# Kernel optimization log

Hardware: AMD Instinct MI355X
Metric: run time of the kernel (lower is better)

Reference implementation:

```python
import jax, jax.numpy as jnp
import numpy as np

NC, NP_, E = 100000, 50000, 500000
DC, DP = 256, 128
HID, OUT = 64, 64
H1, H2 = 2, 1
SLOPE = 0.2


def setup_inputs() -> dict:
    key = jax.random.key(0)
    ks = jax.random.split(key, 32)
    d = {}
    d['x_customer'] = jax.random.normal(ks[0], (NC, DC), jnp.float32)
    d['x_product'] = jax.random.normal(ks[1], (NP_, DP), jnp.float32)
    d['edge_src'] = jax.random.randint(ks[2], (E,), 0, NC, jnp.int32)
    d['edge_dst'] = jax.random.randint(ks[3], (E,), 0, NP_, jnp.int32)
    s = 0.1
    # layer1, edge type (customer, buys, product): src=customer, dst=product
    d['w1b_src'] = jax.random.normal(ks[4], (DC, H1 * HID)) * s
    d['w1b_dst'] = jax.random.normal(ks[5], (DP, H1 * HID)) * s
    d['a1b_src'] = jax.random.normal(ks[6], (H1, HID)) * s
    d['a1b_dst'] = jax.random.normal(ks[7], (H1, HID)) * s
    d['b1b'] = jnp.zeros((H1 * HID,), jnp.float32)
    # layer1, edge type (product, rev_buys, customer): src=product, dst=customer
    d['w1r_src'] = jax.random.normal(ks[8], (DP, H1 * HID)) * s
    d['w1r_dst'] = jax.random.normal(ks[9], (DC, H1 * HID)) * s
    d['a1r_src'] = jax.random.normal(ks[10], (H1, HID)) * s
    d['a1r_dst'] = jax.random.normal(ks[11], (H1, HID)) * s
    d['b1r'] = jnp.zeros((H1 * HID,), jnp.float32)
    # layer2 (input dim = H1*HID = 128 for both node types), heads=1
    d['w2b_src'] = jax.random.normal(ks[12], (H1 * HID, H2 * OUT)) * s
    d['w2b_dst'] = jax.random.normal(ks[13], (H1 * HID, H2 * OUT)) * s
    d['a2b_src'] = jax.random.normal(ks[14], (H2, OUT)) * s
    d['a2b_dst'] = jax.random.normal(ks[15], (H2, OUT)) * s
    d['b2b'] = jnp.zeros((H2 * OUT,), jnp.float32)
    d['w2r_src'] = jax.random.normal(ks[16], (H1 * HID, H2 * OUT)) * s
    d['w2r_dst'] = jax.random.normal(ks[17], (H1 * HID, H2 * OUT)) * s
    d['a2r_src'] = jax.random.normal(ks[18], (H2, OUT)) * s
    d['a2r_dst'] = jax.random.normal(ks[19], (H2, OUT)) * s
    d['b2r'] = jnp.zeros((H2 * OUT,), jnp.float32)
    return d


def _gat_conv(h_src, h_dst, e_src, e_dst, att_src, att_dst, bias, n_dst):
    # h_src: [Ns,H,C] projected source feats; h_dst: [Nd,H,C]
    a_s = (h_src * att_src).sum(-1)  # [Ns,H]
    a_d = (h_dst * att_dst).sum(-1)  # [Nd,H]
    alpha = jax.nn.leaky_relu(a_s[e_src] + a_d[e_dst], negative_slope=SLOPE)  # [E,H]
    m = jax.lax.stop_gradient(jax.ops.segment_max(alpha, e_dst, num_segments=n_dst))
    ex = jnp.exp(alpha - m[e_dst])
    den = jax.ops.segment_sum(ex, e_dst, num_segments=n_dst)
    w = ex / (den[e_dst] + 1e-16)  # segment softmax over incoming edges
    msg = h_src[e_src] * w[..., None]  # [E,H,C]
    out = jax.ops.segment_sum(msg, e_dst, num_segments=n_dst)  # [Nd,H,C]
    return out.reshape(n_dst, -1) + bias


def reference(x_customer, x_product, edge_src, edge_dst,
              w1b_src, w1b_dst, a1b_src, a1b_dst, b1b,
              w1r_src, w1r_dst, a1r_src, a1r_dst, b1r,
              w2b_src, w2b_dst, a2b_src, a2b_dst, b2b,
              w2r_src, w2r_dst, a2r_src, a2r_dst, b2r):
    # ---- layer 1 (heads=2, concat) ----
    hs = (x_customer @ w1b_src).reshape(NC, H1, HID)
    hd = (x_product @ w1b_dst).reshape(NP_, H1, HID)
    p1 = _gat_conv(hs, hd, edge_src, edge_dst, a1b_src, a1b_dst, b1b, NP_)
    hs = (x_product @ w1r_src).reshape(NP_, H1, HID)
    hd = (x_customer @ w1r_dst).reshape(NC, H1, HID)
    c1 = _gat_conv(hs, hd, edge_dst, edge_src, a1r_src, a1r_dst, b1r, NC)
    c1 = jax.nn.relu(c1)
    p1 = jax.nn.relu(p1)
    # ---- layer 2 (heads=1) ----
    hs = (c1 @ w2b_src).reshape(NC, H2, OUT)
    hd = (p1 @ w2b_dst).reshape(NP_, H2, OUT)
    p2 = _gat_conv(hs, hd, edge_src, edge_dst, a2b_src, a2b_dst, b2b, NP_)
    hs = (p1 @ w2r_src).reshape(NP_, H2, OUT)
    hd = (c1 @ w2r_dst).reshape(NC, H2, OUT)
    c2 = _gat_conv(hs, hd, edge_dst, edge_src, a2r_src, a2r_dst, b2r, NC)
    return c2, p2
```

## Files before the change

### kernel.cpp

```cpp
#include <hip/hip_runtime.h>
#include <hip/hip_bf16.h>

typedef __bf16 bf16_t;
typedef bf16_t bf16x2 __attribute__((ext_vector_type(2)));
typedef bf16_t bf16x4 __attribute__((ext_vector_type(4)));
typedef bf16_t bf16x8 __attribute__((ext_vector_type(8)));
typedef float f32x2 __attribute__((ext_vector_type(2)));
typedef float f32x4 __attribute__((ext_vector_type(4)));

static constexpr int NCn = 100000;
static constexpr int NPn = 50000;
static constexpr int NE  = 500000;

__device__ __forceinline__ float ldin(const void* p, size_t i, int fp32) {
    return fp32 ? ((const float*)p)[i] : (float)((const bf16_t*)p)[i];
}

__global__ __launch_bounds__(256) void prep_meta(const void* x, int* flag,
                                                 const void* w1bd, const void* a1bd,
                                                 const void* w1rd, const void* a1rd,
                                                 const void* w2bd, const void* a2bd,
                                                 const void* w2rd, const void* a2rd,
                                                 float* V1bd, float* V1rd,
                                                 float* V2bd, float* V2rd) {
    __shared__ int sflag;
    int t = threadIdx.x;
    if (t < 64) {
        const bf16_t* xb = (const bf16_t*)x;
        int bad = 0;
        for (int i = t; i < 512; i += 64) {
            float v = (float)xb[i];
            if (!(v > -1e4f && v < 1e4f)) bad = 1;
        }
        unsigned long long m = __ballot(bad);
        if (t == 0) { sflag = (m != 0ull) ? 1 : 0; flag[0] = sflag; }
    }
    __syncthreads();
    int fp32 = sflag;
    for (int idx = t; idx < 256; idx += 256) {
        int k = idx >> 1, h = idx & 1;
        float s = 0.f;
        for (int c = 0; c < 64; ++c)
            s += ldin(w1bd, (size_t)k * 128 + h * 64 + c, fp32) * ldin(a1bd, h * 64 + c, fp32);
        V1bd[k * 2 + h] = s;
    }
    for (int idx = t; idx < 512; idx += 256) {
        int k = idx >> 1, h = idx & 1;
        float s = 0.f;
        for (int c = 0; c < 64; ++c)
            s += ldin(w1rd, (size_t)k * 128 + h * 64 + c, fp32) * ldin(a1rd, h * 64 + c, fp32);
        V1rd[k * 2 + h] = s;
    }
    for (int k = t; k < 128; k += 256) {
        float s = 0.f;
        for (int c = 0; c < 64; ++c)
            s += ldin(w2bd, (size_t)k * 64 + c, fp32) * ldin(a2bd, c, fp32);
        V2bd[k] = s;
    }
    for (int k = t; k < 128; k += 256) {
        float s = 0.f;
        for (int c = 0; c < 64; ++c)
            s += ldin(w2rd, (size_t)k * 64 + c, fp32) * ldin(a2rd, c, fp32);
        V2rd[k] = s;
    }
}

__global__ __launch_bounds__(256) void prep_w4(const void* __restrict__ w1b, bf16_t* __restrict__ Wt1b,
                                               const void* __restrict__ w1r, bf16_t* __restrict__ Wt1r,
                                               const void* __restrict__ w2b, bf16_t* __restrict__ Wt2b,
                                               const void* __restrict__ w2r, bf16_t* __restrict__ Wt2r,
                                               const int* __restrict__ flag) {
    int fp32 = flag[0];
    int b = blockIdx.x;
    const void* W; bf16_t* Wt; int N, ks, base;
    if (b < 128)      { W = w1b; Wt = Wt1b; N = 128; ks = 8; base = 0;   }
    else if (b < 192) { W = w1r; Wt = Wt1r; N = 128; ks = 7; base = 128; }
    else if (b < 224) { W = w2b; Wt = Wt2b; N = 64;  ks = 7; base = 192; }
    else              { W = w2r; Wt = Wt2r; N = 64;  ks = 7; base = 224; }
    int idx = (b - base) * 256 + threadIdx.x;
    int K = 1 << ks;
    int n = idx >> ks, k = idx & (K - 1);
    if (n < N) Wt[idx] = (bf16_t)ldin(W, (size_t)k * N + n, fp32);
}

template<int K>
__global__ __launch_bounds__(256) void cvt_rows(const void* __restrict__ X,
                                                bf16_t* __restrict__ Xb,
                                                const float* __restrict__ V,
                                                float* __restrict__ ad,
                                                int M, const int* __restrict__ flag) {
    constexpr int EPL = K / 64;
    int fp32 = flag[0];
    int wid = (blockIdx.x * 256 + threadIdx.x) >> 6;
    int lane = threadIdx.x & 63;
    if (wid >= M) return;
    size_t base = (size_t)wid * K + lane * EPL;
    float x[EPL];
    if constexpr (EPL == 4) {
        if (fp32) { f32x4 t = *(const f32x4*)((const float*)X + base);
#pragma unroll
            for (int j = 0; j < 4; ++j) x[j] = t[j];
        } else { bf16x4 t = *(const bf16x4*)((const bf16_t*)X + base);
#pragma unroll
            for (int j = 0; j < 4; ++j) x[j] = (float)t[j];
        }
        bf16x4 o;
#pragma unroll
        for (int j = 0; j < 4; ++j) o[j] = (bf16_t)x[j];
        *(bf16x4*)(Xb + base) = o;
    } else {
        if (fp32) { f32x2 t = *(const f32x2*)((const float*)X + base);
#pragma unroll
            for (int j = 0; j < 2; ++j) x[j] = t[j];
        } else { bf16x2 t = *(const bf16x2*)((const bf16_t*)X + base);
#pragma unroll
            for (int j = 0; j < 2; ++j) x[j] = (float)t[j];
        }
        bf16x2 o;
#pragma unroll
        for (int j = 0; j < 2; ++j) o[j] = (bf16_t)x[j];
        *(bf16x2*)(Xb + base) = o;
    }
    float a0 = 0.f, a1 = 0.f;
#pragma unroll
    for (int j = 0; j < EPL; ++j) {
        int k = lane * EPL + j;
        a0 += x[j] * V[k * 2];
        a1 += x[j] * V[k * 2 + 1];
    }
    for (int off = 32; off; off >>= 1) {
        a0 += __shfl_down(a0, off);
        a1 += __shfl_down(a1, off);
    }
    if (lane == 0) { ad[(size_t)wid * 2] = a0; ad[(size_t)wid * 2 + 1] = a1; }
}

__global__ __launch_bounds__(256) void zero2(int* __restrict__ a, int na,
                                             int* __restrict__ b, int nb) {
    int i = blockIdx.x * 256 + threadIdx.x;
    if (i < na) a[i] = 0;
    else if (i - na < nb) b[i - na] = 0;
}

__global__ __launch_bounds__(256) void hist2(const int* __restrict__ esrc,
                                             const int* __restrict__ edst,
                                             int* __restrict__ cntR,
                                             int* __restrict__ cntB, int E) {
    int e = blockIdx.x * 256 + threadIdx.x;
    if (e >= E) return;
    atomicAdd(&cntB[edst[e]], 1);
    atomicAdd(&cntR[esrc[e]], 1);
}

__global__ __launch_bounds__(256) void scan_blocks(const int* __restrict__ cnt,
                                                   int* __restrict__ rs,
                                                   int* __restrict__ bsum, int N) {
    int t = threadIdx.x, b = blockIdx.x;
    int base = b * 1024 + t * 4;
    int c[4];
#pragma unroll
    for (int k = 0; k < 4; ++k) { int i = base + k; c[k] = (i < N) ? cnt[i] : 0; }
    int tsum = c[0] + c[1] + c[2] + c[3];
    __shared__ int sd[256];
    sd[t] = tsum;
    __syncthreads();
    for (int off = 1; off < 256; off <<= 1) {
        int x = (t >= off) ? sd[t - off] : 0;
        __syncthreads();
        sd[t] += x;
        __syncthreads();
    }
    int run = sd[t] - tsum;
#pragma unroll
    for (int k = 0; k < 4; ++k) { int i = base + k; if (i < N) rs[i] = run; run += c[k]; }
    if (t == 255) bsum[b] = sd[255];
}

__global__ __launch_bounds__(128) void scan_bsum2(int* __restrict__ bsumB, int nbB,
                                                  int* __restrict__ bsumR, int nbR) {
    int* bsum = blockIdx.x ? bsumR : bsumB;
    int nb = blockIdx.x ? nbR : nbB;
    int t = threadIdx.x;
    __shared__ int sd[128];
    int v = (t < nb) ? bsum[t] : 0;
    sd[t] = v;
    __syncthreads();
    for (int off = 1; off < 128; off <<= 1) {
        int x = (t >= off) ? sd[t - off] : 0;
        __syncthreads();
        sd[t] += x;
        __syncthreads();
    }
    if (t < nb) bsum[t] = sd[t] - v;
}

__global__ __launch_bounds__(256) void scan_add2(int* __restrict__ rsB, const int* __restrict__ bsumB,
                                                 int NB, int* __restrict__ cntB,
                                                 int* __restrict__ rsR, const int* __restrict__ bsumR,
                                                 int NR, int* __restrict__ cntR, int E) {
    int i = blockIdx.x * 256 + threadIdx.x;
    if (i < NB) { int v = rsB[i] + bsumB[i >> 10]; rsB[i] = v; cntB[i] = v; }
    if (i < NR) { int v = rsR[i] + bsumR[i >> 10]; rsR[i] = v; cntR[i] = v; }
    if (i == 0) { rsB[NB] = E; rsR[NR] = E; }
}

__global__ __launch_bounds__(256) void scatter2(const int* __restrict__ esrc,
                                                const int* __restrict__ edst,
                                                int* __restrict__ curB, int* __restrict__ curR,
                                                int* __restrict__ srcsB, int* __restrict__ dstsB,
                                                int* __restrict__ srcsR, int* __restrict__ dstsR,
                                                int E) {
    int e = blockIdx.x * 256 + threadIdx.x;
    if (e >= E) return;
    int s = esrc[e], d = edst[e];
    int pb = atomicAdd(&curB[d], 1);
    srcsB[pb] = s; dstsB[pb] = d;
    int pr = atomicAdd(&curR[s], 1);
    srcsR[pr] = d; dstsR[pr] = s;
}

template<int K>
__global__ __launch_bounds__(256) void gemm_nl(const bf16_t* __restrict__ A,
                                               const bf16_t* __restrict__ Wt,
                                               bf16_t* __restrict__ C,
                                               const void* __restrict__ att,
                                               float* __restrict__ asout, int H,
                                               int M, int N,
                                               const int* __restrict__ flag) {
    const int w = threadIdx.x >> 6;
    const int lane = threadIdx.x & 63;
    const int lm = lane & 15;
    const int lq = lane >> 4;
    const int n0 = blockIdx.y * 64;
    const int r0 = blockIdx.x * 128 + w * 32;
    int ra0 = r0 + lm;       if (ra0 > M - 1) ra0 = M - 1;
    int ra1 = r0 + 16 + lm;  if (ra1 > M - 1) ra1 = M - 1;
    const bf16_t* A0 = A + (size_t)ra0 * K + lq * 8;
    const bf16_t* A1 = A + (size_t)ra1 * K + lq * 8;
    const bf16_t* B0 = Wt + (size_t)(n0 + lm) * K + lq * 8;
    f32x4 acc[2][4] = {};
#pragma unroll
    for (int kt = 0; kt < K / 32; ++kt) {
        bf16x8 a0 = *(const bf16x8*)(A0 + kt * 32);
        bf16x8 a1 = *(const bf16x8*)(A1 + kt * 32);
#pragma unroll
        for (int nt = 0; nt < 4; ++nt) {
            bf16x8 b = *(const bf16x8*)(B0 + (size_t)nt * 16 * K + kt * 32);
            acc[0][nt] = __builtin_amdgcn_mfma_f32_16x16x32_bf16(a0, b, acc[0][nt], 0, 0, 0);
            acc[1][nt] = __builtin_amdgcn_mfma_f32_16x16x32_bf16(a1, b, acc[1][nt], 0, 0, 0);
        }
    }
#pragma unroll
    for (int rt = 0; rt < 2; ++rt) {
        const int crow0 = r0 + rt * 16 + lq * 4;
#pragma unroll
        for (int nt = 0; nt < 4; ++nt) {
            int col = n0 + nt * 16 + lm;
#pragma unroll
            for (int i = 0; i < 4; ++i) {
                int r = crow0 + i;
                if (r < M) C[(size_t)r * N + col] = (bf16_t)acc[rt][nt][i];
            }
        }
    }
    int fp32 = flag[0];
    float attv[4];
#pragma unroll
    for (int nt = 0; nt < 4; ++nt) attv[nt] = ldin(att, n0 + nt * 16 + lm, fp32);
    float part[2][4];
#pragma unroll
    for (int rt = 0; rt < 2; ++rt)
#pragma unroll
        for (int i = 0; i < 4; ++i) {
            float s = 0.f;
#pragma unroll
            for (int nt = 0; nt < 4; ++nt) s += acc[rt][nt][i] * attv[nt];
            part[rt][i] = s;
        }
#pragma unroll
    for (int off = 1; off < 16; off <<= 1)
#pragma unroll
        for (int rt = 0; rt < 2; ++rt)
#pragma unroll
            for (int i = 0; i < 4; ++i)
                part[rt][i] += __shfl_xor(part[rt][i], off);
    if (lm == 0) {
#pragma unroll
        for (int rt = 0; rt < 2; ++rt)
#pragma unroll
            for (int i = 0; i < 4; ++i) {
                int r = r0 + rt * 16 + lq * 4 + i;
                if (r < M) asout[(size_t)r * H + blockIdx.y] = part[rt][i];
            }
    }
}

template<int H>
__global__ __launch_bounds__(256) void edge_ex2(const int* __restrict__ srcsB,
                                                const int* __restrict__ dstsB,
                                                const float* __restrict__ asB,
                                                const float* __restrict__ adB,
                                                float* __restrict__ exBp,
                                                const int* __restrict__ srcsR,
                                                const int* __restrict__ dstsR,
                                                const float* __restrict__ asR,
                                                const float* __restrict__ adR,
                                                float* __restrict__ exRp, int E) {
    int i = blockIdx.x * 256 + threadIdx.x;
    const int *srcs, *dsts; const float *as_, *ad_; float* ex; int j;
    if (i < E) { j = i; srcs = srcsB; dsts = dstsB; as_ = asB; ad_ = adB; ex = exBp; }
    else {
        j = i - E;
        if (j >= E) return;
        srcs = srcsR; dsts = dstsR; as_ = asR; ad_ = adR; ex = exRp;
    }
    int s = srcs[j], d = dsts[j];
    if constexpr (H == 2) {
        f32x2 a = *(const f32x2*)(as_ + 2 * (size_t)s);
        f32x2 b = *(const f32x2*)(ad_ + 2 * (size_t)d);
        float v0 = a[0] + b[0]; v0 = v0 > 0.f ? v0 : 0.2f * v0;
        float v1 = a[1] + b[1]; v1 = v1 > 0.f ? v1 : 0.2f * v1;
        f32x2 o;
        o[0] = __expf(fminf(v0, 60.f));
        o[1] = __expf(fminf(v1, 60.f));
        *(f32x2*)(ex + 2 * (size_t)j) = o;
    } else {
        float v = as_[s] + ad_[d];
        v = v > 0.f ? v : 0.2f * v;
        ex[j] = __expf(fminf(v, 60.f));
    }
}

template<int HD, int MODE>
__global__ __launch_bounds__(256) void aggregate2(
        const int* __restrict__ rsB, const int* __restrict__ srcsB,
        const float* __restrict__ exB, const bf16_t* __restrict__ HmB,
        const void* __restrict__ biasB, const float* __restrict__ V2B,
        float* __restrict__ ad2B, void* __restrict__ outB, size_t obaseB, int NdB,
        const int* __restrict__ rsR, const int* __restrict__ srcsR,
        const float* __restrict__ exR, const bf16_t* __restrict__ HmR,
        const void* __restrict__ biasR, const float* __restrict__ V2R,
        float* __restrict__ ad2R, void* __restrict__ outR, size_t obaseR, int NdR,
        const int* __restrict__ flag) {
    constexpr int NH = HD / 64;
    int gw = (blockIdx.x * 256 + threadIdx.x) >> 6;
    int lane = threadIdx.x & 63;
    const int* rs; const int* srcs; const float* ex; const bf16_t* Hm;
    const void* bias; const float* V2; float* ad2; void* outb; size_t obase; int wid;
    if (gw < NdB) {
        wid = gw;
        rs = rsB; srcs = srcsB; ex = exB; Hm = HmB; bias = biasB;
        V2 = V2B; ad2 = ad2B; outb = outB; obase = obaseB;
    } else {
        wid = gw - NdB;
        if (wid >= NdR) return;
        rs = rsR; srcs = srcsR; ex = exR; Hm = HmR; bias = biasR;
        V2 = V2R; ad2 = ad2R; outb = outR; obase = obaseR;
    }
    int start = rs[wid], end = rs[wid + 1];
    int fp32 = flag[0];
    const int hsel = lane >> 5;

    float den = 0.f, acc0 = 0.f, acc1 = 0.f;
#pragma unroll 4
    for (int j = start; j < end; ++j) {
        int s = srcs[j];
        if constexpr (NH == 2) {
            f32x2 e = *(const f32x2*)(ex + 2 * (size_t)j);
            float eh = hsel ? e[1] : e[0];
            den += eh;
            bf16x2 hv = *(const bf16x2*)(Hm + (size_t)s * 128 + 2 * lane);
            acc0 += (float)hv[0] * eh;
            acc1 += (float)hv[1] * eh;
        } else {
            float eh = ex[j];
            den += eh;
            acc0 += (float)Hm[(size_t)s * 64 + lane] * eh;
        }
    }
    float inv = 1.f / (den + 1e-16f);

    if constexpr (MODE == 0) {
        int c0 = 2 * lane;
        float o0 = fmaxf(acc0 * inv + ldin(bias, c0, fp32), 0.f);
        float o1 = fmaxf(acc1 * inv + ldin(bias, c0 + 1, fp32), 0.f);
        bf16x2 ov;
        ov[0] = (bf16_t)o0;
        ov[1] = (bf16_t)o1;
        *(bf16x2*)((bf16_t*)outb + (size_t)wid * 128 + c0) = ov;
        float pp = o0 * V2[c0] + o1 * V2[c0 + 1];
        for (int off = 32; off; off >>= 1) pp += __shfl_down(pp, off);
        if (lane == 0) ad2[wid] = pp;
    } else {
        float o = acc0 * inv + ldin(bias, lane, fp32);
        size_t oi = obase + (size_t)wid * 64 + lane;
        if (fp32) ((float*)outb)[oi] = o;
        else      ((bf16_t*)outb)[oi] = (bf16_t)o;
    }
}

extern "C" void kernel_launch(void* const* d_in, const int* in_sizes, int n_in,
                              void* d_out, int out_size, void* d_ws, size_t ws_size,
                              hipStream_t stream) {
    const void* xc = d_in[0];
    const void* xp = d_in[1];
    const int* esrc = (const int*)d_in[2];
    const int* edst = (const int*)d_in[3];
    const void* w1b_src = d_in[4];
    const void* w1b_dst = d_in[5];
    const void* a1b_src = d_in[6];
    const void* a1b_dst = d_in[7];
    const void* b1b     = d_in[8];
    const void* w1r_src = d_in[9];
    const void* w1r_dst = d_in[10];
    const void* a1r_src = d_in[11];
    const void* a1r_dst = d_in[12];
    const void* b1r     = d_in[13];
    const void* w2b_src = d_in[14];
    const void* w2b_dst = d_in[15];
    const void* a2b_src = d_in[16];
    const void* a2b_dst = d_in[17];
    const void* b2b     = d_in[18];
    const void* w2r_src = d_in[19];
    const void* w2r_dst = d_in[20];
    const void* a2r_src = d_in[21];
    const void* a2r_dst = d_in[22];
    const void* b2r     = d_in[23];

    char* p = (char*)d_ws;
    auto alloc = [&](size_t nbytes) {
        char* r = p;
        p += (nbytes + 255) & ~(size_t)255;
        return r;
    };
    int* flag   = (int*)alloc(256);
    float* V1bd = (float*)alloc(256 * 4);
    float* V1rd = (float*)alloc(512 * 4);
    float* V2bd = (float*)alloc(128 * 4);
    float* V2rd = (float*)alloc(128 * 4);
    bf16_t* Wt1b = (bf16_t*)alloc(128 * 256 * 2);
    bf16_t* Wt1r = (bf16_t*)alloc(128 * 128 * 2);
    bf16_t* Wt2b = (bf16_t*)alloc(64 * 128 * 2);
    bf16_t* Wt2r = (bf16_t*)alloc(64 * 128 * 2);
    float* as_b = (float*)alloc((size_t)NCn * 2 * 4);
    float* as_r = (float*)alloc((size_t)NPn * 2 * 4);
    float* as2_c = (float*)alloc((size_t)NCn * 4);
    float* as2_p = (float*)alloc((size_t)NPn * 4);
    float* ad_b = (float*)alloc((size_t)NPn * 2 * 4);
    float* ad_r = (float*)alloc((size_t)NCn * 2 * 4);
    float* ad2_b = (float*)alloc((size_t)NPn * 4);
    float* ad2_r = (float*)alloc((size_t)NCn * 4);
    int* rsB    = (int*)alloc((size_t)(NPn + 1) * 4);
    int* rsR    = (int*)alloc((size_t)(NCn + 1) * 4);
    int* srcsB  = (int*)alloc((size_t)NE * 4);
    int* srcsR  = (int*)alloc((size_t)NE * 4);
    int* dstsB  = (int*)alloc((size_t)NE * 4);
    int* dstsR  = (int*)alloc((size_t)NE * 4);
    float* exB  = (float*)alloc((size_t)NE * 2 * 4);
    float* exR  = (float*)alloc((size_t)NE * 2 * 4);
    int* cntB   = (int*)alloc((size_t)NPn * 4);
    int* cntR   = (int*)alloc((size_t)NCn * 4);
    int* bsumB  = (int*)alloc(128 * 4);
    int* bsumR  = (int*)alloc(128 * 4);
    bf16_t* xcb = (bf16_t*)alloc((size_t)NCn * 256 * 2);
    bf16_t* xpb = (bf16_t*)alloc((size_t)NPn * 128 * 2);
    bf16_t* Hc  = (bf16_t*)alloc((size_t)NCn * 128 * 2);
    bf16_t* Hp  = (bf16_t*)alloc((size_t)NPn * 128 * 2);
    bf16_t* c1  = (bf16_t*)alloc((size_t)NCn * 128 * 2);
    bf16_t* p1  = (bf16_t*)alloc((size_t)NPn * 128 * 2);
    bf16_t* Hc2 = (bf16_t*)alloc((size_t)NCn * 64 * 2);
    bf16_t* Hp2 = (bf16_t*)alloc((size_t)NPn * 64 * 2);

    const dim3 blk(256);
    const int gE = (NE + 255) / 256;
    const int g2E = (2 * NE + 255) / 256;
    const int sbP = (NPn + 1023) / 1024;
    const int sbR = (NCn + 1023) / 1024;
    const int gmC = (NCn + 127) / 128;
    const int gmP = (NPn + 127) / 128;
    const int gNC = (NCn + 255) / 256;
    const int gBoth = (NPn + NCn + 255) / 256;
    const int gAgg = (NPn + NCn + 3) / 4;

    prep_meta<<<1, 256, 0, stream>>>(xc, flag, w1b_dst, a1b_dst, w1r_dst, a1r_dst,
                                     w2b_dst, a2b_dst, w2r_dst, a2r_dst,
                                     V1bd, V1rd, V2bd, V2rd);
    prep_w4<<<256, blk, 0, stream>>>(w1b_src, Wt1b, w1r_src, Wt1r,
                                     w2b_src, Wt2b, w2r_src, Wt2r, flag);

    zero2<<<gBoth, blk, 0, stream>>>(cntB, NPn, cntR, NCn);
    hist2<<<gE, blk, 0, stream>>>(esrc, edst, cntR, cntB, NE);
    scan_blocks<<<sbP, blk, 0, stream>>>(cntB, rsB, bsumB, NPn);
    scan_blocks<<<sbR, blk, 0, stream>>>(cntR, rsR, bsumR, NCn);
    scan_bsum2<<<2, 128, 0, stream>>>(bsumB, sbP, bsumR, sbR);
    scan_add2<<<gNC, blk, 0, stream>>>(rsB, bsumB, NPn, cntB, rsR, bsumR, NCn, cntR, NE);
    scatter2<<<gE, blk, 0, stream>>>(esrc, edst, cntB, cntR, srcsB, dstsB, srcsR, dstsR, NE);

    cvt_rows<256><<<(NCn + 3) / 4, blk, 0, stream>>>(xc, xcb, V1rd, ad_r, NCn, flag);
    cvt_rows<128><<<(NPn + 3) / 4, blk, 0, stream>>>(xp, xpb, V1bd, ad_b, NPn, flag);

    gemm_nl<256><<<dim3(gmC, 2), blk, 0, stream>>>(xcb, Wt1b, Hc, a1b_src, as_b, 2, NCn, 128, flag);
    gemm_nl<128><<<dim3(gmP, 2), blk, 0, stream>>>(xpb, Wt1r, Hp, a1r_src, as_r, 2, NPn, 128, flag);

    edge_ex2<2><<<g2E, blk, 0, stream>>>(srcsB, dstsB, as_b, ad_b, exB,
                                         srcsR, dstsR, as_r, ad_r, exR, NE);
    aggregate2<128, 0><<<gAgg, blk, 0, stream>>>(
        rsB, srcsB, exB, Hc, b1b, V2bd, ad2_b, p1, 0, NPn,
        rsR, srcsR, exR, Hp, b1r, V2rd, ad2_r, c1, 0, NCn, flag);

    gemm_nl<128><<<dim3(gmC, 1), blk, 0, stream>>>(c1, Wt2b, Hc2, a2b_src, as2_c, 1, NCn, 64, flag);
    gemm_nl<128><<<dim3(gmP, 1), blk, 0, stream>>>(p1, Wt2r, Hp2, a2r_src, as2_p, 1, NPn, 64, flag);

    edge_ex2<1><<<g2E, blk, 0, stream>>>(srcsB, dstsB, as2_c, ad2_b, exB,
                                         srcsR, dstsR, as2_p, ad2_r, exR, NE);
    aggregate2<64, 1><<<gAgg, blk, 0, stream>>>(
        rsB, srcsB, exB, Hc2, b2b, nullptr, nullptr, d_out, (size_t)NCn * 64, NPn,
        rsR, srcsR, exR, Hp2, b2r, nullptr, nullptr, d_out, 0, NCn, flag);
}
```

Baseline: 622.9 us.

## Merge paired launches and pack source offsets with edge weights for aggregation

Paired kernels for the two edge types (scan, row conversion, layer-1 and layer-2 GEMMs) are merged into single launches that pick their branch from the block index, cutting launch count and tail idle time. The edge-weight pass now also writes the precomputed byte offset of each source row into a packed record next to the exp weights. Aggregation then reads one vector load per edge instead of separate srcs and ex loads. In exchange the packed buffer is larger (16 bytes per edge for two heads, including padding) and the offset is bit-cast into a float slot.

Result: faster. 598.1 us (-4.0%).

```diff
diff --git a/kernel.cpp b/kernel.cpp
--- a/kernel.cpp
+++ b/kernel.cpp
@@ -84,14 +84,13 @@
 }
 
 template<int K>
-__global__ __launch_bounds__(256) void cvt_rows(const void* __restrict__ X,
-                                                bf16_t* __restrict__ Xb,
-                                                const float* __restrict__ V,
-                                                float* __restrict__ ad,
-                                                int M, const int* __restrict__ flag) {
+__device__ __forceinline__ void cvt_body(const void* __restrict__ X,
+                                         bf16_t* __restrict__ Xb,
+                                         const float* __restrict__ V,
+                                         float* __restrict__ ad,
+                                         int M, int fp32, int blk) {
     constexpr int EPL = K / 64;
-    int fp32 = flag[0];
-    int wid = (blockIdx.x * 256 + threadIdx.x) >> 6;
+    int wid = (blk * 256 + (int)threadIdx.x) >> 6;
     int lane = threadIdx.x & 63;
     if (wid >= M) return;
     size_t base = (size_t)wid * K + lane * EPL;
@@ -133,6 +132,16 @@
         a1 += __shfl_down(a1, off);
     }
     if (lane == 0) { ad[(size_t)wid * 2] = a0; ad[(size_t)wid * 2 + 1] = a1; }
+}
+
+__global__ __launch_bounds__(256) void cvt2(const void* __restrict__ Xc, bf16_t* __restrict__ Xcb,
+                                            const float* __restrict__ Vc, float* __restrict__ adc,
+                                            const void* __restrict__ Xp, bf16_t* __restrict__ Xpb,
+                                            const float* __restrict__ Vp, float* __restrict__ adp,
+                                            int gC, const int* __restrict__ flag) {
+    int fp32 = flag[0];
+    if ((int)blockIdx.x < gC) cvt_body<256>(Xc, Xcb, Vc, adc, NCn, fp32, blockIdx.x);
+    else                      cvt_body<128>(Xp, Xpb, Vp, adp, NPn, fp32, blockIdx.x - gC);
 }
 
 __global__ __launch_bounds__(256) void zero2(int* __restrict__ a, int na,
@@ -152,10 +161,14 @@
     atomicAdd(&cntR[esrc[e]], 1);
 }
 
-__global__ __launch_bounds__(256) void scan_blocks(const int* __restrict__ cnt,
-                                                   int* __restrict__ rs,
-                                                   int* __restrict__ bsum, int N) {
-    int t = threadIdx.x, b = blockIdx.x;
+__global__ __launch_bounds__(256) void scan_blocks2(const int* __restrict__ cntB, int* __restrict__ rsB,
+                                                    int* __restrict__ bsumB, int NB, int sbB,
+                                                    const int* __restrict__ cntR, int* __restrict__ rsR,
+                                                    int* __restrict__ bsumR, int NR) {
+    const int* cnt; int* rs; int* bsum; int N; int b;
+    if ((int)blockIdx.x < sbB) { cnt = cntB; rs = rsB; bsum = bsumB; N = NB; b = blockIdx.x; }
+    else { cnt = cntR; rs = rsR; bsum = bsumR; N = NR; b = blockIdx.x - sbB; }
+    int t = threadIdx.x;
     int base = b * 1024 + t * 4;
     int c[4];
 #pragma unroll
@@ -220,19 +233,18 @@
 }
 
 template<int K>
-__global__ __launch_bounds__(256) void gemm_nl(const bf16_t* __restrict__ A,
-                                               const bf16_t* __restrict__ Wt,
-                                               bf16_t* __restrict__ C,
-                                               const void* __restrict__ att,
-                                               float* __restrict__ asout, int H,
-                                               int M, int N,
-                                               const int* __restrict__ flag) {
+__device__ __forceinline__ void gemm_body(const bf16_t* __restrict__ A,
+                                          const bf16_t* __restrict__ Wt,
+                                          bf16_t* __restrict__ C,
+                                          const void* __restrict__ att,
+                                          float* __restrict__ asout, int H,
+                                          int M, int N, int fp32, int bx, int by) {
     const int w = threadIdx.x >> 6;
     const int lane = threadIdx.x & 63;
     const int lm = lane & 15;
     const int lq = lane >> 4;
-    const int n0 = blockIdx.y * 64;
-    const int r0 = blockIdx.x * 128 + w * 32;
+    const int n0 = by * 64;
+    const int r0 = bx * 128 + w * 32;
     int ra0 = r0 + lm;       if (ra0 > M - 1) ra0 = M - 1;
     int ra1 = r0 + 16 + lm;  if (ra1 > M - 1) ra1 = M - 1;
     const bf16_t* A0 = A + (size_t)ra0 * K + lq * 8;
@@ -263,7 +275,6 @@
             }
         }
     }
-    int fp32 = flag[0];
     float attv[4];
 #pragma unroll
     for (int nt = 0; nt < 4; ++nt) attv[nt] = ldin(att, n0 + nt * 16 + lm, fp32);
@@ -290,29 +301,53 @@
 #pragma unroll
             for (int i = 0; i < 4; ++i) {
                 int r = r0 + rt * 16 + lq * 4 + i;
-                if (r < M) asout[(size_t)r * H + blockIdx.y] = part[rt][i];
+                if (r < M) asout[(size_t)r * H + by] = part[rt][i];
             }
     }
 }
 
+__global__ __launch_bounds__(256) void gemm_l1(const bf16_t* __restrict__ xcb, const bf16_t* __restrict__ Wt1b,
+                                               bf16_t* __restrict__ Hc, const void* __restrict__ a1b, float* __restrict__ as_b,
+                                               const bf16_t* __restrict__ xpb, const bf16_t* __restrict__ Wt1r,
+                                               bf16_t* __restrict__ Hp, const void* __restrict__ a1r, float* __restrict__ as_r,
+                                               int gmC, const int* __restrict__ flag) {
+    int fp32 = flag[0];
+    if ((int)blockIdx.x < gmC)
+        gemm_body<256>(xcb, Wt1b, Hc, a1b, as_b, 2, NCn, 128, fp32, blockIdx.x, blockIdx.y);
+    else
+        gemm_body<128>(xpb, Wt1r, Hp, a1r, as_r, 2, NPn, 128, fp32, blockIdx.x - gmC, blockIdx.y);
+}
+
+__global__ __launch_bounds__(256) void gemm_l2(const bf16_t* __restrict__ c1, const bf16_t* __restrict__ Wt2b,
+                                               bf16_t* __restrict__ Hc2, const void* __restrict__ a2b, float* __restrict__ as2c,
+                                               const bf16_t* __restrict__ p1, const bf16_t* __restrict__ Wt2r,
+                                               bf16_t* __restrict__ Hp2, const void* __restrict__ a2r, float* __restrict__ as2p,
+                                               int gmC, const int* __restrict__ flag) {
+    int fp32 = flag[0];
+    if ((int)blockIdx.x < gmC)
+        gemm_body<128>(c1, Wt2b, Hc2, a2b, as2c, 1, NCn, 64, fp32, blockIdx.x, 0);
+    else
+        gemm_body<128>(p1, Wt2r, Hp2, a2r, as2p, 1, NPn, 64, fp32, blockIdx.x - gmC, 0);
+}
+
 template<int H>
-__global__ __launch_bounds__(256) void edge_ex2(const int* __restrict__ srcsB,
+__global__ __launch_bounds__(256) void edge_pk2(const int* __restrict__ srcsB,
                                                 const int* __restrict__ dstsB,
                                                 const float* __restrict__ asB,
                                                 const float* __restrict__ adB,
-                                                float* __restrict__ exBp,
+                                                float* __restrict__ pkB,
                                                 const int* __restrict__ srcsR,
                                                 const int* __restrict__ dstsR,
                                                 const float* __restrict__ asR,
                                                 const float* __restrict__ adR,
-                                                float* __restrict__ exRp, int E) {
+                                                float* __restrict__ pkR, int E) {
     int i = blockIdx.x * 256 + threadIdx.x;
-    const int *srcs, *dsts; const float *as_, *ad_; float* ex; int j;
-    if (i < E) { j = i; srcs = srcsB; dsts = dstsB; as_ = asB; ad_ = adB; ex = exBp; }
+    const int *srcs, *dsts; const float *as_, *ad_; float* pk; int j;
+    if (i < E) { j = i; srcs = srcsB; dsts = dstsB; as_ = asB; ad_ = adB; pk = pkB; }
     else {
         j = i - E;
         if (j >= E) return;
-        srcs = srcsR; dsts = dstsR; as_ = asR; ad_ = adR; ex = exRp;
+        srcs = srcsR; dsts = dstsR; as_ = asR; ad_ = adR; pk = pkR;
     }
     int s = srcs[j], d = dsts[j];
     if constexpr (H == 2) {
@@ -320,41 +355,46 @@
         f32x2 b = *(const f32x2*)(ad_ + 2 * (size_t)d);
         float v0 = a[0] + b[0]; v0 = v0 > 0.f ? v0 : 0.2f * v0;
         float v1 = a[1] + b[1]; v1 = v1 > 0.f ? v1 : 0.2f * v1;
-        f32x2 o;
-        o[0] = __expf(fminf(v0, 60.f));
-        o[1] = __expf(fminf(v1, 60.f));
-        *(f32x2*)(ex + 2 * (size_t)j) = o;
+        f32x4 o;
+        o[0] = __uint_as_float((unsigned)s << 8);
+        o[1] = __expf(fminf(v0, 60.f));
+        o[2] = __expf(fminf(v1, 60.f));
+        o[3] = 0.f;
+        *(f32x4*)(pk + 4 * (size_t)j) = o;
     } else {
         float v = as_[s] + ad_[d];
         v = v > 0.f ? v : 0.2f * v;
-        ex[j] = __expf(fminf(v, 60.f));
+        f32x2 o;
+        o[0] = __uint_as_float((unsigned)s << 7);
+        o[1] = __expf(fminf(v, 60.f));
+        *(f32x2*)(pk + 2 * (size_t)j) = o;
     }
 }
 
 template<int HD, int MODE>
 __global__ __launch_bounds__(256) void aggregate2(
-        const int* __restrict__ rsB, const int* __restrict__ srcsB,
-        const float* __restrict__ exB, const bf16_t* __restrict__ HmB,
-        const void* __restrict__ biasB, const float* __restrict__ V2B,
-        float* __restrict__ ad2B, void* __restrict__ outB, size_t obaseB, int NdB,
-        const int* __restrict__ rsR, const int* __restrict__ srcsR,
-        const float* __restrict__ exR, const bf16_t* __restrict__ HmR,
-        const void* __restrict__ biasR, const float* __restrict__ V2R,
-        float* __restrict__ ad2R, void* __restrict__ outR, size_t obaseR, int NdR,
+        const int* __restrict__ rsB, const float* __restrict__ pkB,
+        const bf16_t* __restrict__ HmB, const void* __restrict__ biasB,
+        const float* __restrict__ V2B, float* __restrict__ ad2B,
+        void* __restrict__ outB, size_t obaseB, int NdB,
+        const int* __restrict__ rsR, const float* __restrict__ pkR,
+        const bf16_t* __restrict__ HmR, const void* __restrict__ biasR,
+        const float* __restrict__ V2R, float* __restrict__ ad2R,
+        void* __restrict__ outR, size_t obaseR, int NdR,
         const int* __restrict__ flag) {
     constexpr int NH = HD / 64;
     int gw = (blockIdx.x * 256 + threadIdx.x) >> 6;
     int lane = threadIdx.x & 63;
-    const int* rs; const int* srcs; const float* ex; const bf16_t* Hm;
+    const int* rs; const float* pk; const bf16_t* Hm;
     const void* bias; const float* V2; float* ad2; void* outb; size_t obase; int wid;
     if (gw < NdB) {
         wid = gw;
-        rs = rsB; srcs = srcsB; ex = exB; Hm = HmB; bias = biasB;
+        rs = rsB; pk = pkB; Hm = HmB; bias = biasB;
         V2 = V2B; ad2 = ad2B; outb = outB; obase = obaseB;
     } else {
         wid = gw - NdB;
         if (wid >= NdR) return;
-        rs = rsR; srcs = srcsR; ex = exR; Hm = HmR; bias = biasR;
+        rs = rsR; pk = pkR; Hm = HmR; bias = biasR;
         V2 = V2R; ad2 = ad2R; outb = outR; obase = obaseR;
     }
     int start = rs[wid], end = rs[wid + 1];
@@ -362,20 +402,29 @@
     const int hsel = lane >> 5;
 
     float den = 0.f, acc0 = 0.f, acc1 = 0.f;
+    if constexpr (NH == 2) {
+        const char* Hlane = (const char*)Hm + 4 * lane;
+        const f32x4* pkv = (const f32x4*)pk;
 #pragma unroll 4
-    for (int j = start; j < end; ++j) {
-        int s = srcs[j];
-        if constexpr (NH == 2) {
-            f32x2 e = *(const f32x2*)(ex + 2 * (size_t)j);
-            float eh = hsel ? e[1] : e[0];
+        for (int j = start; j < end; ++j) {
+            f32x4 e = pkv[j];
+            unsigned off = __float_as_uint(e[0]);
+            float eh = hsel ? e[2] : e[1];
             den += eh;
-            bf16x2 hv = *(const bf16x2*)(Hm + (size_t)s * 128 + 2 * lane);
+            bf16x2 hv = *(const bf16x2*)(Hlane + off);
             acc0 += (float)hv[0] * eh;
             acc1 += (float)hv[1] * eh;
-        } else {
-            float eh = ex[j];
+        }
+    } else {
+        const char* Hlane = (const char*)Hm + 2 * lane;
+        const f32x2* pkv = (const f32x2*)pk;
+#pragma unroll 4
+        for (int j = start; j < end; ++j) {
+            f32x2 e = pkv[j];
+            unsigned off = __float_as_uint(e[0]);
+            float eh = e[1];
             den += eh;
-            acc0 += (float)Hm[(size_t)s * 64 + lane] * eh;
+            acc0 += (float)(*(const bf16_t*)(Hlane + off)) * eh;
         }
     }
     float inv = 1.f / (den + 1e-16f);
@@ -456,8 +505,8 @@
     int* srcsR  = (int*)alloc((size_t)NE * 4);
     int* dstsB  = (int*)alloc((size_t)NE * 4);
     int* dstsR  = (int*)alloc((size_t)NE * 4);
-    float* exB  = (float*)alloc((size_t)NE * 2 * 4);
-    float* exR  = (float*)alloc((size_t)NE * 2 * 4);
+    float* pkB  = (float*)alloc((size_t)NE * 16);
+    float* pkR  = (float*)alloc((size_t)NE * 16);
     int* cntB   = (int*)alloc((size_t)NPn * 4);
     int* cntR   = (int*)alloc((size_t)NCn * 4);
     int* bsumB  = (int*)alloc(128 * 4);
@@ -481,6 +530,8 @@
     const int gNC = (NCn + 255) / 256;
     const int gBoth = (NPn + NCn + 255) / 256;
     const int gAgg = (NPn + NCn + 3) / 4;
+    const int gCvtC = (NCn + 3) / 4;
+    const int gCvtP = (NPn + 3) / 4;
 
     prep_meta<<<1, 256, 0, stream>>>(xc, flag, w1b_dst, a1b_dst, w1r_dst, a1r_dst,
                                      w2b_dst, a2b_dst, w2r_dst, a2r_dst,
@@ -490,30 +541,32 @@
 
     zero2<<<gBoth, blk, 0, stream>>>(cntB, NPn, cntR, NCn);
     hist2<<<gE, blk, 0, stream>>>(esrc, edst, cntR, cntB, NE);
-    scan_blocks<<<sbP, blk, 0, stream>>>(cntB, rsB, bsumB, NPn);
-    scan_blocks<<<sbR, blk, 0, stream>>>(cntR, rsR, bsumR, NCn);
+    scan_blocks2<<<sbP + sbR, blk, 0, stream>>>(cntB, rsB, bsumB, NPn, sbP,
+                                                cntR, rsR, bsumR, NCn);
     scan_bsum2<<<2, 128, 0, stream>>>(bsumB, sbP, bsumR, sbR);
     scan_add2<<<gNC, blk, 0, stream>>>(rsB, bsumB, NPn, cntB, rsR, bsumR, NCn, cntR, NE);
     scatter2<<<gE, blk, 0, stream>>>(esrc, edst, cntB, cntR, srcsB, dstsB, srcsR, dstsR, NE);
 
-    cvt_rows<256><<<(NCn + 3) / 4, blk, 0, stream>>>(xc, xcb, V1rd, ad_r, NCn, flag);
-    cvt_rows<128><<<(NPn + 3) / 4, blk, 0, stream>>>(xp, xpb, V1bd, ad_b, NPn, flag);
-
-    gemm_nl<256><<<dim3(gmC, 2), blk, 0, stream>>>(xcb, Wt1b, Hc, a1b_src, as_b, 2, NCn, 128, flag);
-    gemm_nl<128><<<dim3(gmP, 2), blk, 0, stream>>>(xpb, Wt1r, Hp, a1r_src, as_r, 2, NPn, 128, flag);
-
-    edge_ex2<2><<<g2E, blk, 0, stream>>>(srcsB, dstsB, as_b, ad_b, exB,
-                                         srcsR, dstsR, as_r, ad_r, exR, NE);
+    cvt2<<<gCvtC + gCvtP, blk, 0, stream>>>(xc, xcb, V1rd, ad_r,
+                                            xp, xpb, V1bd, ad_b, gCvtC, flag);
+
+    gemm_l1<<<dim3(gmC + gmP, 2), blk, 0, stream>>>(xcb, Wt1b, Hc, a1b_src, as_b,
+                                                    xpb, Wt1r, Hp, a1r_src, as_r,
+                                                    gmC, flag);
+
+    edge_pk2<2><<<g2E, blk, 0, stream>>>(srcsB, dstsB, as_b, ad_b, pkB,
+                                         srcsR, dstsR, as_r, ad_r, pkR, NE);
     aggregate2<128, 0><<<gAgg, blk, 0, stream>>>(
-        rsB, srcsB, exB, Hc, b1b, V2bd, ad2_b, p1, 0, NPn,
-        rsR, srcsR, exR, Hp, b1r, V2rd, ad2_r, c1, 0, NCn, flag);
-
-    gemm_nl<128><<<dim3(gmC, 1), blk, 0, stream>>>(c1, Wt2b, Hc2, a2b_src, as2_c, 1, NCn, 64, flag);
-    gemm_nl<128><<<dim3(gmP, 1), blk, 0, stream>>>(p1, Wt2r, Hp2, a2r_src, as2_p, 1, NPn, 64, flag);
-
-    edge_ex2<1><<<g2E, blk, 0, stream>>>(srcsB, dstsB, as2_c, ad2_b, exB,
-                                         srcsR, dstsR, as2_p, ad2_r, exR, NE);
+        rsB, pkB, Hc, b1b, V2bd, ad2_b, p1, 0, NPn,
+        rsR, pkR, Hp, b1r, V2rd, ad2_r, c1, 0, NCn, flag);
+
+    gemm_l2<<<dim3(gmC + gmP, 1), blk, 0, stream>>>(c1, Wt2b, Hc2, a2b_src, as2_c,
+                                                    p1, Wt2r, Hp2, a2r_src, as2_p,
+                                                    gmC, flag);
+
+    edge_pk2<1><<<g2E, blk, 0, stream>>>(srcsB, dstsB, as2_c, ad2_b, pkB,
+                                         srcsR, dstsR, as2_p, ad2_r, pkR, NE);
     aggregate2<64, 1><<<gAgg, blk, 0, stream>>>(
-        rsB, srcsB, exB, Hc2, b2b, nullptr, nullptr, d_out, (size_t)NCn * 64, NPn,
-        rsR, srcsR, exR, Hp2, b2r, nullptr, nullptr, d_out, 0, NCn, flag);
-}
+        rsB, pkB, Hc2, b2b, nullptr, nullptr, d_out, (size_t)NCn * 64, NPn,
+        rsR, pkR, Hp2, b2r, nullptr, nullptr, d_out, 0, NCn, flag);
+}
```
